# Performance work log

Hardware: AMD Instinct MI355X
Metric: run time of the kernel (lower is better)

## Reference

```python
import jax, jax.numpy as jnp
import numpy as np

N_NODES = 100000
N_EDGES = 800000
F_IN, HID, N_CLS = 256, 128, 32


def setup_inputs() -> dict:
    key = jax.random.key(0)
    k1, k2, k3, k4, k5 = jax.random.split(key, 5)
    features = jax.random.normal(k1, (N_NODES, F_IN), dtype=jnp.float32)
    # random directed edges with no self loops (so add_remaining_self_loops == append all loops)
    src = jax.random.randint(k2, (N_EDGES,), 0, N_NODES)
    off = jax.random.randint(k3, (N_EDGES,), 1, N_NODES)
    dst = (src + off) % N_NODES
    edge_index = jnp.stack([src, dst]).astype(jnp.int64)
    # Glorot-style params for the two GCNConv layers
    W1 = jax.random.normal(k4, (F_IN, HID), dtype=jnp.float32) * (1.0 / np.sqrt(F_IN))
    b1 = jnp.zeros((HID,), dtype=jnp.float32)
    W2 = jax.random.normal(k5, (HID, N_CLS), dtype=jnp.float32) * (1.0 / np.sqrt(HID))
    b2 = jnp.zeros((N_CLS,), dtype=jnp.float32)
    return {"features": features, "edge_index": edge_index, "W1": W1, "b1": b1, "W2": W2, "b2": b2}


def _gcn_conv(x, W, b, src, dst, norm, n):
    xw = x @ W                                  # [N, d_out] dense GEMM
    msg = xw[src] * norm[:, None]               # gather + scale, [E, d_out]
    out = jax.ops.segment_sum(msg, dst, num_segments=n)  # scatter-add to targets
    return out + b


def reference(features, edge_index, W1, b1, W2, b2):
    n = features.shape[0]
    # add_remaining_self_loops (input has none, so append all)
    loops = jnp.arange(n, dtype=edge_index.dtype)
    src = jnp.concatenate([edge_index[0], loops])
    dst = jnp.concatenate([edge_index[1], loops])
    # gcn_norm: deg over targets, sym normalization deg^-1/2 A deg^-1/2
    deg = jax.ops.segment_sum(jnp.ones_like(src, dtype=features.dtype), dst, num_segments=n)
    dinv = jnp.where(deg > 0, jax.lax.rsqrt(deg), 0.0)
    norm = dinv[src] * dinv[dst]
    x = _gcn_conv(features, W1, b1, src, dst, norm, n)
    x = jax.nn.relu(x)
    # dropout is identity at inference (training=False)
    x = _gcn_conv(x, W2, b2, src, dst, norm, n)
    return jax.nn.log_softmax(x, axis=1)
```

## Files before the change

### kernel.cpp

```cpp
#include <hip/hip_runtime.h>
#include <hip/hip_bf16.h>

typedef __bf16 bf16_t;
typedef __attribute__((ext_vector_type(8))) __bf16 bf16x8;
typedef __attribute__((ext_vector_type(4))) float f32x4;
typedef __attribute__((ext_vector_type(2))) float f32x2;

#define RANGES 32
#define SLICES 16

__device__ inline void packB_one(const float* __restrict__ B, bf16_t* __restrict__ Bp,
                                 int N, int idx) {
    int j    = idx & 7;
    int lane = (idx >> 3) & 63;
    int st   = idx >> 9;
    int nt   = N >> 4;
    int s = st / nt, t = st - s * nt;
    int k = s * 32 + (lane >> 4) * 8 + j;
    int n = t * 16 + (lane & 15);
    Bp[idx] = (bf16_t)B[(size_t)k * N + n];
}

__device__ inline void fma8_fp8(uint2 u, float w, float* a) {
    f32x2 p;
    p = __builtin_amdgcn_cvt_pk_f32_fp8(u.x, false); a[0] += p[0] * w; a[1] += p[1] * w;
    p = __builtin_amdgcn_cvt_pk_f32_fp8(u.x, true);  a[2] += p[0] * w; a[3] += p[1] * w;
    p = __builtin_amdgcn_cvt_pk_f32_fp8(u.y, false); a[4] += p[0] * w; a[5] += p[1] * w;
    p = __builtin_amdgcn_cvt_pk_f32_fp8(u.y, true);  a[6] += p[0] * w; a[7] += p[1] * w;
}

__global__ __launch_bounds__(256) void k_prep(
        const float* __restrict__ W1, bf16_t* __restrict__ Bp1,
        const float* __restrict__ W2, bf16_t* __restrict__ Bp2) {
    int idx = blockIdx.x * 256 + threadIdx.x;
    if (idx < 32768) packB_one(W1, Bp1, 128, idx);
    else             packB_one(W2, Bp2, 32, idx - 32768);
}

template <int KSTEPS, int NTILES>
__global__ __launch_bounds__(256) void k_front(
        const float* __restrict__ feat, const bf16_t* __restrict__ Bp1,
        unsigned char* __restrict__ XW1, int M,
        const int* __restrict__ dst, int* __restrict__ degS,
        int* __restrict__ rank, int Nn, int E, int DEGB) {
    int b = blockIdx.x, t = threadIdx.x;
    if (b < DEGB) {
        __shared__ int hist[3200];
        const int CHUNK = (Nn + RANGES - 1) / RANGES;
        int r = b >> 4, s = b & (SLICES - 1);
        int base = r * CHUNK;
        int top  = min(base + CHUNK, Nn);
        int len  = top - base;
        for (int i = t; i < len; i += 256) hist[i] = 0;
        __syncthreads();
        int tag = s << 24;
        int sliceLen = ((E + (SLICES * 4 - 1)) / (SLICES * 4)) * 4;
        int e0 = s * sliceLen;
        int e1 = min(e0 + sliceLen, E);
        for (int i = e0 + t * 4; i < e1; i += 1024) {
            if (i + 4 <= e1) {
                int4 v = *(const int4*)(dst + i);
                if (v.x >= base && v.x < top) rank[i]     = tag | atomicAdd(&hist[v.x - base], 1);
                if (v.y >= base && v.y < top) rank[i + 1] = tag | atomicAdd(&hist[v.y - base], 1);
                if (v.z >= base && v.z < top) rank[i + 2] = tag | atomicAdd(&hist[v.z - base], 1);
                if (v.w >= base && v.w < top) rank[i + 3] = tag | atomicAdd(&hist[v.w - base], 1);
            } else {
                for (int j = 0; j < 4 && i + j < e1; ++j) {
                    int d = dst[i + j];
                    if (d >= base && d < top) rank[i + j] = tag | atomicAdd(&hist[d - base], 1);
                }
            }
        }
        __syncthreads();
        int* dplane = degS + (size_t)s * Nn + base;
        for (int i = t; i < len; i += 256) dplane[i] = hist[i];
        return;
    }
    b -= DEGB;
    {
        int wave = (b * 256 + t) >> 6;
        if (wave * 16 >= M) return;
        int lane = t & 63;
        int r16 = lane & 15, quad = lane >> 4;
        const int K = KSTEPS * 32, N = NTILES * 16;
        f32x4 acc[NTILES] = {};
        const float* arow = feat + (size_t)(wave * 16 + r16) * K + quad * 8;
#pragma unroll
        for (int s = 0; s < KSTEPS; ++s) {
            const float* ap = arow + s * 32;
            bf16x8 a;
#pragma unroll
            for (int j = 0; j < 8; ++j) a[j] = (bf16_t)ap[j];
            const bf16_t* bp = Bp1 + ((size_t)(s * NTILES) * 64 + lane) * 8;
#pragma unroll
            for (int tt = 0; tt < NTILES; ++tt) {
                bf16x8 bb = *(const bf16x8*)(bp + tt * 512);
                acc[tt] = __builtin_amdgcn_mfma_f32_16x16x32_bf16(a, bb, acc[tt], 0, 0, 0);
            }
        }
#pragma unroll
        for (int tt = 0; tt < NTILES; ++tt)
#pragma unroll
            for (int r = 0; r < 4; ++r) {
                int pk = __builtin_amdgcn_cvt_pk_fp8_f32(acc[tt][r], acc[tt][r], 0, false);
                XW1[(size_t)(wave * 16 + quad * 4 + r) * N + tt * 16 + r16] =
                    (unsigned char)pk;
            }
    }
}

__global__ __launch_bounds__(256) void k_dinv_scan1(
        const int* __restrict__ degS, int* __restrict__ degTot,
        int* __restrict__ off, float* __restrict__ dinv,
        int* __restrict__ bsum, int n) {
    __shared__ int red[256];
    int b = blockIdx.x, t = threadIdx.x;
    int base = b * 1024 + t * 4;
    int s = 0;
#pragma unroll
    for (int j = 0; j < 4; ++j) {
        int i = base + j;
        if (i < n) {
            int run = 0;
#pragma unroll
            for (int x = 0; x < SLICES; ++x) {
                int v = degS[(size_t)x * n + i];
                off[(size_t)x * n + i] = run;
                run += v;
            }
            degTot[i] = run;
            s += run;
            dinv[i] = rsqrtf((float)(run + 1));
        }
    }
    red[t] = s;
    __syncthreads();
    for (int d = 128; d > 0; d >>= 1) {
        if (t < d) red[t] += red[t + d];
        __syncthreads();
    }
    if (t == 0) bsum[b] = red[0];
}

__global__ __launch_bounds__(256) void k_scan3f(const int* __restrict__ degTot,
                                                const int* __restrict__ bsum, int nb,
                                                int* __restrict__ rowPtr, int n) {
    __shared__ int red[256];
    __shared__ int boff[256];
    int b = blockIdx.x, t = threadIdx.x;
    int base = b * 1024 + t * 4;
    int v[4]; int s = 0;
#pragma unroll
    for (int j = 0; j < 4; ++j) { int i = base + j; v[j] = (i < n) ? degTot[i] : 0; s += v[j]; }
    red[t] = s;
    boff[t] = (t < nb) ? bsum[t] : 0;
    __syncthreads();
    for (int d = 1; d < 256; d <<= 1) {
        int u  = (t >= d) ? red[t - d]  : 0;
        int u2 = (t >= d) ? boff[t - d] : 0;
        __syncthreads();
        red[t] += u;
        boff[t] += u2;
        __syncthreads();
    }
    int blockOff = (b == 0) ? 0 : boff[b - 1];
    if (b == 0 && t == 0) rowPtr[n] = boff[nb - 1];
    int run = blockOff + red[t] - s;
#pragma unroll
    for (int j = 0; j < 4; ++j) {
        int i = base + j;
        if (i < n) { rowPtr[i] = run; run += v[j]; }
    }
}

__global__ __launch_bounds__(256) void k_scatter(
        const int* __restrict__ src, const int* __restrict__ dst,
        const int* __restrict__ rank, const int* __restrict__ rowPtr,
        const int* __restrict__ off, const float* __restrict__ dinv,
        int2* __restrict__ edata, int Nn, int E) {
    int i = (blockIdx.x * 256 + threadIdx.x) * 4;
    if (i + 4 <= E) {
        int4 s4 = *(const int4*)(src + i);
        int4 d4 = *(const int4*)(dst + i);
        int4 r4 = *(const int4*)(rank + i);
        int p0 = rowPtr[d4.x] + off[(size_t)(((unsigned)r4.x) >> 24) * Nn + d4.x] + (r4.x & 0x00FFFFFF);
        int p1 = rowPtr[d4.y] + off[(size_t)(((unsigned)r4.y) >> 24) * Nn + d4.y] + (r4.y & 0x00FFFFFF);
        int p2 = rowPtr[d4.z] + off[(size_t)(((unsigned)r4.z) >> 24) * Nn + d4.z] + (r4.z & 0x00FFFFFF);
        int p3 = rowPtr[d4.w] + off[(size_t)(((unsigned)r4.w) >> 24) * Nn + d4.w] + (r4.w & 0x00FFFFFF);
        int2 e0; e0.x = s4.x; e0.y = __float_as_int(dinv[s4.x] * dinv[d4.x]);
        int2 e1; e1.x = s4.y; e1.y = __float_as_int(dinv[s4.y] * dinv[d4.y]);
        int2 e2; e2.x = s4.z; e2.y = __float_as_int(dinv[s4.z] * dinv[d4.z]);
        int2 e3; e3.x = s4.w; e3.y = __float_as_int(dinv[s4.w] * dinv[d4.w]);
        edata[p0] = e0; edata[p1] = e1; edata[p2] = e2; edata[p3] = e3;
    } else {
        for (int j = 0; j < 4; ++j) {
            int e = i + j;
            if (e >= E) break;
            int s = src[e], d = dst[e];
            int r = rank[e];
            int2 p; p.x = s; p.y = __float_as_int(dinv[s] * dinv[d]);
            edata[rowPtr[d] + off[(size_t)(((unsigned)r) >> 24) * Nn + d] + (r & 0x00FFFFFF)] = p;
        }
    }
}

template <int KSTEPS, int NTILES>
__global__ __launch_bounds__(256) void k_gemm_p(
        const bf16_t* __restrict__ Ap, const bf16_t* __restrict__ Bp,
        bf16_t* __restrict__ C, int M) {
    int wave = (blockIdx.x * blockDim.x + threadIdx.x) >> 6;
    if (wave * 16 >= M) return;
    int lane = threadIdx.x & 63;
    int r16 = lane & 15, quad = lane >> 4;
    const int N = NTILES * 16;
    f32x4 acc[NTILES] = {};
    const bf16_t* apb = Ap + (size_t)wave * (KSTEPS * 512) + lane * 8;
#pragma unroll
    for (int s = 0; s < KSTEPS; ++s) {
        bf16x8 a = *(const bf16x8*)(apb + s * 512);
        const bf16_t* bp = Bp + ((size_t)(s * NTILES) * 64 + lane) * 8;
#pragma unroll
        for (int t = 0; t < NTILES; ++t) {
            bf16x8 b = *(const bf16x8*)(bp + t * 512);
            acc[t] = __builtin_amdgcn_mfma_f32_16x16x32_bf16(a, b, acc[t], 0, 0, 0);
        }
    }
#pragma unroll
    for (int t = 0; t < NTILES; ++t)
#pragma unroll
        for (int r = 0; r < 4; ++r)
            C[(size_t)(wave * 16 + quad * 4 + r) * N + t * 16 + r16] = (bf16_t)acc[t][r];
}

__global__ __launch_bounds__(256) void k_agg1(
        const int* __restrict__ rowPtr, const int2* __restrict__ edata,
        const unsigned char* __restrict__ XW1, const float* __restrict__ dinv,
        const float* __restrict__ b1, bf16_t* __restrict__ Hp, int n) {
    int wave = (blockIdx.x * blockDim.x + threadIdx.x) >> 6;
    if (wave >= n) return;
    int lane = threadIdx.x & 63;
    int fl = (lane & 15) << 3;
    int h  = lane >> 4;
    int r0 = rowPtr[wave], r1 = rowPtr[wave + 1];
    float d = dinv[wave], d2 = d * d;
    uint2 us = *(const uint2*)(XW1 + (size_t)wave * 128 + fl);
    float a0[8] = {}, a1[8] = {};
    int k = r0 + h;
    for (; k + 4 < r1; k += 8) {
        int2 e0 = edata[k], e1 = edata[k + 4];
        float w0 = __int_as_float(e0.y), w1 = __int_as_float(e1.y);
        uint2 u0 = *(const uint2*)(XW1 + (size_t)e0.x * 128 + fl);
        uint2 u1 = *(const uint2*)(XW1 + (size_t)e1.x * 128 + fl);
        fma8_fp8(u0, w0, a0);
        fma8_fp8(u1, w1, a1);
    }
    if (k < r1) {
        int2 e0 = edata[k];
        float w0 = __int_as_float(e0.y);
        uint2 u0 = *(const uint2*)(XW1 + (size_t)e0.x * 128 + fl);
        fma8_fp8(u0, w0, a0);
    }
#pragma unroll
    for (int j = 0; j < 8; ++j) {
        a0[j] += a1[j];
        a0[j] += __shfl_xor(a0[j], 16);
        a0[j] += __shfl_xor(a0[j], 32);
    }
    if (h == 0) {
        fma8_fp8(us, d2, a0);
        bf16x8 hv;
#pragma unroll
        for (int j = 0; j < 8; ++j) {
            float v = a0[j] + b1[fl + j];
            hv[j] = (bf16_t)fmaxf(v, 0.f);
        }
        int q = lane & 15;
        size_t off2 = (((size_t)(wave >> 4) * 4 + (q >> 2)) * 64
                       + (wave & 15) + 16 * (q & 3)) * 8;
        *(bf16x8*)(Hp + off2) = hv;
    }
}

__global__ __launch_bounds__(256) void k_agg2(
        const int* __restrict__ rowPtr, const int2* __restrict__ edata,
        const bf16_t* __restrict__ XW2, const float* __restrict__ dinv,
        const float* __restrict__ b2, float* __restrict__ out, int n) {
    int wave = (blockIdx.x * blockDim.x + threadIdx.x) >> 6;
    if (wave >= n) return;
    int lane = threadIdx.x & 63;
    int g = lane & 15;
    int h = lane >> 4;
    int r0 = rowPtr[wave], r1 = rowPtr[wave + 1];
    float d = dinv[wave], d2 = d * d;
    unsigned ps = *(const unsigned*)(XW2 + ((size_t)wave << 5) + 2 * g);
    float2 bb = *(const float2*)(b2 + 2 * g);
    float a00 = 0.f, a01 = 0.f, a10 = 0.f, a11 = 0.f;
    int k = r0 + h;
    for (; k + 4 < r1; k += 8) {
        int2 e0 = edata[k], e1 = edata[k + 4];
        float w0 = __int_as_float(e0.y), w1 = __int_as_float(e1.y);
        unsigned p0 = *(const unsigned*)(XW2 + ((size_t)e0.x << 5) + 2 * g);
        unsigned p1 = *(const unsigned*)(XW2 + ((size_t)e1.x << 5) + 2 * g);
        a00 += __int_as_float(p0 << 16) * w0;
        a01 += __int_as_float(p0 & 0xffff0000u) * w0;
        a10 += __int_as_float(p1 << 16) * w1;
        a11 += __int_as_float(p1 & 0xffff0000u) * w1;
    }
    if (k < r1) {
        int2 e0 = edata[k];
        float w0 = __int_as_float(e0.y);
        unsigned p0 = *(const unsigned*)(XW2 + ((size_t)e0.x << 5) + 2 * g);
        a00 += __int_as_float(p0 << 16) * w0;
        a01 += __int_as_float(p0 & 0xffff0000u) * w0;
    }
    float v0 = a00 + a10, v1 = a01 + a11;
    v0 += __shfl_xor(v0, 16); v0 += __shfl_xor(v0, 32);
    v1 += __shfl_xor(v1, 16); v1 += __shfl_xor(v1, 32);
    v0 += __int_as_float(ps << 16) * d2 + bb.x;
    v1 += __int_as_float(ps & 0xffff0000u) * d2 + bb.y;
    float mx = fmaxf(v0, v1);
#pragma unroll
    for (int m = 8; m >= 1; m >>= 1) mx = fmaxf(mx, __shfl_xor(mx, m));
    float s = __expf(v0 - mx) + __expf(v1 - mx);
#pragma unroll
    for (int m = 8; m >= 1; m >>= 1) s += __shfl_xor(s, m);
    if (h == 0) {
        float ls = __logf(s);
        float2 o; o.x = v0 - mx - ls; o.y = v1 - mx - ls;
        *(float2*)(out + ((size_t)wave << 5) + 2 * g) = o;
    }
}

extern "C" void kernel_launch(void* const* d_in, const int* in_sizes, int n_in,
                              void* d_out, int out_size, void* d_ws, size_t ws_size,
                              hipStream_t stream) {
    const float* feat = (const float*)d_in[0];
    const int*   eidx = (const int*)d_in[1];
    const float* W1   = (const float*)d_in[2];
    const float* b1   = (const float*)d_in[3];
    const float* W2   = (const float*)d_in[4];
    const float* b2   = (const float*)d_in[5];
    float* out = (float*)d_out;

    const int FIN = 256, HID = 128, NCLS = 32;
    const int N = in_sizes[0] / FIN;
    const int E = in_sizes[1] / 2;
    const int* src = eidx;
    const int* dst = eidx + E;

    char* ws = (char*)d_ws;
    size_t o = 0;
    auto alloc = [&](size_t bytes) -> void* {
        void* p = ws + o;
        o = (o + bytes + 255) & ~(size_t)255;
        return p;
    };
    int*    degS   = (int*)   alloc((size_t)SLICES * N * 4);
    int*    offA   = (int*)   alloc((size_t)SLICES * N * 4);
    int*    degTot = (int*)   alloc((size_t)N * 4);
    int*    rank   = (int*)   alloc((size_t)E * 4);
    float*  dinv   = (float*) alloc((size_t)N * 4);
    int*    rowPtr = (int*)   alloc((size_t)(N + 1) * 4);
    int*    bsum   = (int*)   alloc(256 * 4);
    bf16_t* Bp1    = (bf16_t*)alloc((size_t)(FIN / 32) * (HID / 16) * 512 * 2);
    bf16_t* Bp2    = (bf16_t*)alloc((size_t)(HID / 32) * (NCLS / 16) * 512 * 2);
    int2*   edata  = (int2*)  alloc((size_t)E * 8);
    unsigned char* XW1 = (unsigned char*)alloc((size_t)N * HID);
    bf16_t* Hp     = (bf16_t*)alloc((size_t)N * HID * 2);
    bf16_t* XW2    = (bf16_t*)XW1;

    const int T = 256;
    const int NB = (N + 1023) >> 10;
    const int DEGB  = RANGES * SLICES;
    const int GEMMB = (((N + 15) / 16) * 64 + T - 1) / T;
    const int PACKB = (32768 + 4096) / 256;

    k_prep      <<<PACKB, T, 0, stream>>>(W1, Bp1, W2, Bp2);
    k_front<8, 8><<<DEGB + GEMMB, T, 0, stream>>>(
        feat, Bp1, XW1, N, dst, degS, rank, N, E, DEGB);
    k_dinv_scan1<<<NB, T, 0, stream>>>(degS, degTot, offA, dinv, bsum, N);
    k_scan3f    <<<NB, T, 0, stream>>>(degTot, bsum, NB, rowPtr, N);
    k_scatter   <<<(E + 1023) / 1024, T, 0, stream>>>(
        src, dst, rank, rowPtr, offA, dinv, edata, N, E);
    k_agg1<<<(N * 64 + T - 1) / T, T, 0, stream>>>(rowPtr, edata, XW1, dinv, b1, Hp, N);
    {
        int waves = (N + 15) / 16;
        k_gemm_p<4, 2><<<(waves * 64 + T - 1) / T, T, 0, stream>>>(Hp, Bp2, XW2, N);
    }
    k_agg2<<<(N * 64 + T - 1) / T, T, 0, stream>>>(rowPtr, edata, XW2, dinv, b2, out, N);
}
```

Baseline: 311.6 us.

## Fuse second-layer GEMM into layer-1 aggregation via shared-memory strip

The layer-1 aggregation kernel now runs 16 nodes per 1024-thread block and writes their ReLU'd hidden rows into a shared-memory strip. One wave then does the 128x32 MFMA GEMM on that strip and writes XW2 directly. This removes the separate GEMM launch and the bf16 hidden-matrix round trip through global memory. The cost is a block-wide barrier that makes the whole block wait for its slowest node. While one wave does the GEMM, the other 15 waves sit idle, and the large blocks may reduce scheduling flexibility.

Result: slower. 318.2 us (+2.1%).

```diff
diff --git a/kernel.cpp b/kernel.cpp
--- a/kernel.cpp
+++ b/kernel.cpp
@@ -204,80 +204,77 @@
     }
 }
 
-template <int KSTEPS, int NTILES>
-__global__ __launch_bounds__(256) void k_gemm_p(
-        const bf16_t* __restrict__ Ap, const bf16_t* __restrict__ Bp,
-        bf16_t* __restrict__ C, int M) {
-    int wave = (blockIdx.x * blockDim.x + threadIdx.x) >> 6;
-    if (wave * 16 >= M) return;
-    int lane = threadIdx.x & 63;
-    int r16 = lane & 15, quad = lane >> 4;
-    const int N = NTILES * 16;
-    f32x4 acc[NTILES] = {};
-    const bf16_t* apb = Ap + (size_t)wave * (KSTEPS * 512) + lane * 8;
-#pragma unroll
-    for (int s = 0; s < KSTEPS; ++s) {
-        bf16x8 a = *(const bf16x8*)(apb + s * 512);
-        const bf16_t* bp = Bp + ((size_t)(s * NTILES) * 64 + lane) * 8;
-#pragma unroll
-        for (int t = 0; t < NTILES; ++t) {
-            bf16x8 b = *(const bf16x8*)(bp + t * 512);
-            acc[t] = __builtin_amdgcn_mfma_f32_16x16x32_bf16(a, b, acc[t], 0, 0, 0);
-        }
-    }
-#pragma unroll
-    for (int t = 0; t < NTILES; ++t)
-#pragma unroll
-        for (int r = 0; r < 4; ++r)
-            C[(size_t)(wave * 16 + quad * 4 + r) * N + t * 16 + r16] = (bf16_t)acc[t][r];
-}
-
-__global__ __launch_bounds__(256) void k_agg1(
+__global__ __launch_bounds__(1024) void k_agg1(
         const int* __restrict__ rowPtr, const int2* __restrict__ edata,
         const unsigned char* __restrict__ XW1, const float* __restrict__ dinv,
-        const float* __restrict__ b1, bf16_t* __restrict__ Hp, int n) {
-    int wave = (blockIdx.x * blockDim.x + threadIdx.x) >> 6;
-    if (wave >= n) return;
+        const float* __restrict__ b1, const bf16_t* __restrict__ Bp2,
+        bf16_t* __restrict__ XW2, int n) {
+    __shared__ bf16_t hstrip[16][128];
+    int w    = threadIdx.x >> 6;
     int lane = threadIdx.x & 63;
+    int strip = blockIdx.x;
+    int node  = strip * 16 + w;
     int fl = (lane & 15) << 3;
     int h  = lane >> 4;
-    int r0 = rowPtr[wave], r1 = rowPtr[wave + 1];
-    float d = dinv[wave], d2 = d * d;
-    uint2 us = *(const uint2*)(XW1 + (size_t)wave * 128 + fl);
-    float a0[8] = {}, a1[8] = {};
-    int k = r0 + h;
-    for (; k + 4 < r1; k += 8) {
-        int2 e0 = edata[k], e1 = edata[k + 4];
-        float w0 = __int_as_float(e0.y), w1 = __int_as_float(e1.y);
-        uint2 u0 = *(const uint2*)(XW1 + (size_t)e0.x * 128 + fl);
-        uint2 u1 = *(const uint2*)(XW1 + (size_t)e1.x * 128 + fl);
-        fma8_fp8(u0, w0, a0);
-        fma8_fp8(u1, w1, a1);
-    }
-    if (k < r1) {
-        int2 e0 = edata[k];
-        float w0 = __int_as_float(e0.y);
-        uint2 u0 = *(const uint2*)(XW1 + (size_t)e0.x * 128 + fl);
-        fma8_fp8(u0, w0, a0);
-    }
-#pragma unroll
-    for (int j = 0; j < 8; ++j) {
-        a0[j] += a1[j];
-        a0[j] += __shfl_xor(a0[j], 16);
-        a0[j] += __shfl_xor(a0[j], 32);
-    }
-    if (h == 0) {
-        fma8_fp8(us, d2, a0);
-        bf16x8 hv;
+    if (node < n) {
+        int r0 = rowPtr[node], r1 = rowPtr[node + 1];
+        float d = dinv[node], d2 = d * d;
+        uint2 us = *(const uint2*)(XW1 + (size_t)node * 128 + fl);
+        float a0[8] = {}, a1[8] = {};
+        int k = r0 + h;
+        for (; k + 4 < r1; k += 8) {
+            int2 e0 = edata[k], e1 = edata[k + 4];
+            float w0 = __int_as_float(e0.y), w1 = __int_as_float(e1.y);
+            uint2 u0 = *(const uint2*)(XW1 + (size_t)e0.x * 128 + fl);
+            uint2 u1 = *(const uint2*)(XW1 + (size_t)e1.x * 128 + fl);
+            fma8_fp8(u0, w0, a0);
+            fma8_fp8(u1, w1, a1);
+        }
+        if (k < r1) {
+            int2 e0 = edata[k];
+            float w0 = __int_as_float(e0.y);
+            uint2 u0 = *(const uint2*)(XW1 + (size_t)e0.x * 128 + fl);
+            fma8_fp8(u0, w0, a0);
+        }
 #pragma unroll
         for (int j = 0; j < 8; ++j) {
-            float v = a0[j] + b1[fl + j];
-            hv[j] = (bf16_t)fmaxf(v, 0.f);
-        }
-        int q = lane & 15;
-        size_t off2 = (((size_t)(wave >> 4) * 4 + (q >> 2)) * 64
-                       + (wave & 15) + 16 * (q & 3)) * 8;
-        *(bf16x8*)(Hp + off2) = hv;
+            a0[j] += a1[j];
+            a0[j] += __shfl_xor(a0[j], 16);
+            a0[j] += __shfl_xor(a0[j], 32);
+        }
+        if (h == 0) {
+            fma8_fp8(us, d2, a0);
+            bf16x8 hv;
+#pragma unroll
+            for (int j = 0; j < 8; ++j) {
+                float v = a0[j] + b1[fl + j];
+                hv[j] = (bf16_t)fmaxf(v, 0.f);
+            }
+            *(bf16x8*)(&hstrip[w][fl]) = hv;
+        }
+    }
+    __syncthreads();
+    if (threadIdx.x < 64) {
+        int r16 = lane & 15, quad = lane >> 4;
+        f32x4 acc[2] = {};
+#pragma unroll
+        for (int s = 0; s < 4; ++s) {
+            bf16x8 a = *(const bf16x8*)(&hstrip[r16][s * 32 + quad * 8]);
+            const bf16_t* bp = Bp2 + ((size_t)(s * 2) * 64 + lane) * 8;
+#pragma unroll
+            for (int t = 0; t < 2; ++t) {
+                bf16x8 b = *(const bf16x8*)(bp + t * 512);
+                acc[t] = __builtin_amdgcn_mfma_f32_16x16x32_bf16(a, b, acc[t], 0, 0, 0);
+            }
+        }
+#pragma unroll
+        for (int t = 0; t < 2; ++t)
+#pragma unroll
+            for (int r = 0; r < 4; ++r) {
+                int row = strip * 16 + quad * 4 + r;
+                if (row < n)
+                    XW2[(size_t)row * 32 + t * 16 + r16] = (bf16_t)acc[t][r];
+            }
     }
 }
 
@@ -366,8 +363,7 @@
     bf16_t* Bp2    = (bf16_t*)alloc((size_t)(HID / 32) * (NCLS / 16) * 512 * 2);
     int2*   edata  = (int2*)  alloc((size_t)E * 8);
     unsigned char* XW1 = (unsigned char*)alloc((size_t)N * HID);
-    bf16_t* Hp     = (bf16_t*)alloc((size_t)N * HID * 2);
-    bf16_t* XW2    = (bf16_t*)XW1;
+    bf16_t* XW2    = (bf16_t*)alloc((size_t)N * NCLS * 2);
 
     const int T = 256;
     const int NB = (N + 1023) >> 10;
@@ -382,10 +378,7 @@
     k_scan3f    <<<NB, T, 0, stream>>>(degTot, bsum, NB, rowPtr, N);
     k_scatter   <<<(E + 1023) / 1024, T, 0, stream>>>(
         src, dst, rank, rowPtr, offA, dinv, edata, N, E);
-    k_agg1<<<(N * 64 + T - 1) / T, T, 0, stream>>>(rowPtr, edata, XW1, dinv, b1, Hp, N);
-    {
-        int waves = (N + 15) / 16;
-        k_gemm_p<4, 2><<<(waves * 64 + T - 1) / T, T, 0, stream>>>(Hp, Bp2, XW2, N);
-    }
+    k_agg1<<<(N + 15) / 16, 1024, 0, stream>>>(
+        rowPtr, edata, XW1, dinv, b1, Bp2, XW2, N);
     k_agg2<<<(N * 64 + T - 1) / T, T, 0, stream>>>(rowPtr, edata, XW2, dinv, b2, out, N);
 }
```
